# Kernel tuning notes

Hardware: AMD Instinct MI355X
Metric: run time of the kernel (lower is better)

The kernel has to match this reference:

```python
import jax, jax.numpy as jnp
import numpy as np

K, D, S, H = 8, 2, 1, 12  # kernel_size, dilation, stride, h_size


def setup_inputs() -> dict:
    key = jax.random.key(0)
    k1, k2 = jax.random.split(key)
    x = jax.random.normal(k1, (32, 2048, 64), dtype=jnp.float32)
    A = jax.random.normal(k2, (64, H, H), dtype=jnp.float32) * 0.1
    return {"x": x, "A": A}


def reference(x, A):
    B, T, C = x.shape
    pad = (K + (K - 1) * (D - 1) - 1) // 2  # = 7
    # replicate padding along time
    xp = jnp.pad(x, ((0, 0), (pad, pad), (0, 0)), mode='edge')  # (B, Tp, C)
    Tp = xp.shape[1]
    seg = (Tp - (K - 1) * D - 1) // S + 1
    # dilated unfold: gather overlapping windows along time
    idx = jnp.arange(seg)[:, None] * S + jnp.arange(K)[None, :] * D  # (seg, K)
    win = xp[:, idx, :]                       # (B, seg, K, C)
    w = win.reshape(B * seg, K, C)            # (N, K, C)
    # path increments within each window
    dx = w[:, 1:, :] - w[:, :-1, :]           # (N, K-1, C)
    # skew-symmetric (so(n)) parametrisation of the Lie-algebra map
    Ask = A - jnp.swapaxes(A, -1, -2)         # (C, H, H)
    M = jnp.einsum('nkc,chw->nkhw', dx, Ask)  # (N, K-1, H, H)
    # matrix exponential of each increment's Lie-algebra element
    E = jax.vmap(jax.scipy.linalg.expm)(M.reshape(-1, H, H)).reshape(M.shape)
    # sequential development: z_{t+1} = z_t @ exp(M_t), z_0 = I
    z0 = jnp.broadcast_to(jnp.eye(H, dtype=x.dtype), (B * seg, H, H))

    def step(z, e):
        return jnp.matmul(z, e), None

    zT, _ = jax.lax.scan(step, z0, jnp.swapaxes(E, 0, 1))  # scan over K-1 steps
    dev = zT.reshape(B, seg, H * H)
    sp = w[:, 0, :].reshape(B, seg, C)        # start point of each partition
    return jnp.concatenate([dev, sp], axis=-1)  # (B, seg, H*H + C)
```

## Files before the change

### kernel.cpp

```cpp
#include <hip/hip_runtime.h>

#define B_ 32
#define T_ 2048
#define C_ 64
#define NP_ 2060
#define MSTRIDE 144
#define LSTRIDE 148

typedef short short8_t __attribute__((ext_vector_type(8)));
typedef float f32x4 __attribute__((ext_vector_type(4)));

__device__ __forceinline__ unsigned short f2bf(float f) {
  unsigned u = __float_as_uint(f);
  return (unsigned short)((u + 0x7FFFu + ((u >> 16) & 1u)) >> 16);
}
__device__ __forceinline__ float bf2f(unsigned short s) {
  return __uint_as_float(((unsigned)s) << 16);
}

__global__ __launch_bounds__(256) void k1_mfma(const float* __restrict__ x,
                                               const float* __restrict__ A,
                                               float* __restrict__ M) {
  __shared__ unsigned int askw[9216];
  const int b = blockIdx.y;
  const int p0 = blockIdx.x * 64;
  const int tid = threadIdx.x;
  const float sc = 1.0f / 32.0f;

  for (int P = tid; P < 4608; P += 256) {
    const int j2 = P & 3;
    const int col = (P >> 2) & 15;
    const int koct = (P >> 6) & 3;
    const int rest = P >> 8;
    const int tile = rest % 9;
    const int ks = rest / 9;
    const int e = tile * 16 + col;
    const int h = e / 12, w = e - h * 12;
    const int c0 = ks * 32 + koct * 8 + j2 * 2;
    const float v0 = (A[c0 * 144 + e] - A[c0 * 144 + w * 12 + h]) * sc;
    const float v1 = (A[(c0 + 1) * 144 + e] - A[(c0 + 1) * 144 + w * 12 + h]) * sc;
    const unsigned short h0 = f2bf(v0), h1 = f2bf(v1);
    const unsigned short l0 = f2bf(v0 - bf2f(h0)), l1 = f2bf(v1 - bf2f(h1));
    const int widx = (((ks * 9 + tile) * 4 + koct) * 16 + col) * 4 + j2;
    askw[widx] = ((unsigned)h1 << 16) | h0;
    askw[4608 + widx] = ((unsigned)l1 << 16) | l0;
  }
  __syncthreads();

  const int wv = tid >> 6;
  const int lane = tid & 63;
  const int mrow = lane & 15;
  const int koct = lane >> 4;
  const int p = p0 + wv * 16 + mrow;
  const int i1 = min(max(p - 7, 0), T_ - 1);
  const int i2 = min(max(p - 5, 0), T_ - 1);
  const float* xb = x + (size_t)b * T_ * C_;

  short8_t ah[2], al[2];
#pragma unroll
  for (int ks = 0; ks < 2; ++ks) {
    const int c0 = ks * 32 + koct * 8;
    const float4 u1a = *(const float4*)(xb + (size_t)i1 * C_ + c0);
    const float4 u1b = *(const float4*)(xb + (size_t)i1 * C_ + c0 + 4);
    const float4 u2a = *(const float4*)(xb + (size_t)i2 * C_ + c0);
    const float4 u2b = *(const float4*)(xb + (size_t)i2 * C_ + c0 + 4);
    float d[8];
    d[0] = u2a.x - u1a.x; d[1] = u2a.y - u1a.y;
    d[2] = u2a.z - u1a.z; d[3] = u2a.w - u1a.w;
    d[4] = u2b.x - u1b.x; d[5] = u2b.y - u1b.y;
    d[6] = u2b.z - u1b.z; d[7] = u2b.w - u1b.w;
#pragma unroll
    for (int j = 0; j < 8; ++j) {
      const unsigned short hs = f2bf(d[j]);
      ah[ks][j] = (short)hs;
      al[ks][j] = (short)f2bf(d[j] - bf2f(hs));
    }
  }

  float* Mb = M + (size_t)b * NP_ * MSTRIDE;
  const int dcol = lane & 15;
  const int pbase = p0 + wv * 16 + (lane >> 4) * 4;
  const char* lds = (const char*)askw;
#pragma unroll
  for (int tile = 0; tile < 9; ++tile) {
    f32x4 acc = {0.f, 0.f, 0.f, 0.f};
#pragma unroll
    for (int ks = 0; ks < 2; ++ks) {
      const int fb = (((ks * 9 + tile) * 4 + koct) * 16 + dcol) * 16;
      const short8_t bh = *(const short8_t*)(lds + fb);
      const short8_t bl = *(const short8_t*)(lds + 18432 + fb);
      acc = __builtin_amdgcn_mfma_f32_16x16x32_bf16(ah[ks], bh, acc, 0, 0, 0);
      acc = __builtin_amdgcn_mfma_f32_16x16x32_bf16(ah[ks], bl, acc, 0, 0, 0);
      acc = __builtin_amdgcn_mfma_f32_16x16x32_bf16(al[ks], bh, acc, 0, 0, 0);
    }
#pragma unroll
    for (int reg = 0; reg < 4; ++reg) {
      const int pr = pbase + reg;
      if (pr < NP_) Mb[(size_t)pr * MSTRIDE + tile * 16 + dcol] = acc[reg];
    }
  }
}

template <int Q>
__device__ __forceinline__ float qb(float v) {
  return __int_as_float(
      __builtin_amdgcn_mov_dpp(__float_as_int(v), Q * 0x55, 0xf, 0xf, true));
}

template <bool ACC>
__device__ __forceinline__ void qmm_t(const float a[3][12], const float b[3][12],
                                      float c[3][12]) {
  if (!ACC) {
#pragma unroll
    for (int i = 0; i < 3; ++i)
#pragma unroll
      for (int j = 0; j < 12; ++j) c[i][j] = 0.f;
  }
#define QMM_K(OWNER, E)                                                  \
  {                                                                      \
    float bk[12];                                                        \
    _Pragma("unroll")                                                    \
    for (int j = 0; j < 12; ++j) bk[j] = qb<OWNER>(b[E][j]);             \
    _Pragma("unroll")                                                    \
    for (int i = 0; i < 3; ++i) {                                        \
      const float av = a[i][3 * OWNER + E];                              \
      _Pragma("unroll")                                                  \
      for (int j = 0; j < 12; ++j) c[i][j] = fmaf(av, bk[j], c[i][j]);   \
    }                                                                    \
  }
  QMM_K(0, 0) QMM_K(0, 1) QMM_K(0, 2)
  QMM_K(1, 0) QMM_K(1, 1) QMM_K(1, 2)
  QMM_K(2, 0) QMM_K(2, 1) QMM_K(2, 2)
  QMM_K(3, 0) QMM_K(3, 1) QMM_K(3, 2)
#undef QMM_K
}
__device__ __forceinline__ void qmm(const float a[3][12], const float b[3][12],
                                    float c[3][12]) { qmm_t<false>(a, b, c); }
__device__ __forceinline__ void qmma(const float a[3][12], const float b[3][12],
                                     float c[3][12]) { qmm_t<true>(a, b, c); }

__global__ __launch_bounds__(256) void k2_expm(float* __restrict__ M) {
  const int gq = (blockIdx.x * 256 + threadIdx.x) >> 2;
  const int r = threadIdx.x & 3;
  float* gp = M + (size_t)gq * MSTRIDE + 36 * r;

  float a[3][12], t2[3][12], t3[3][12];
#pragma unroll
  for (int i = 0; i < 3; ++i)
#pragma unroll
    for (int q4 = 0; q4 < 3; ++q4) {
      float4 v = *(const float4*)(gp + i * 12 + q4 * 4);
      a[i][q4 * 4 + 0] = v.x;
      a[i][q4 * 4 + 1] = v.y;
      a[i][q4 * 4 + 2] = v.z;
      a[i][q4 * 4 + 3] = v.w;
    }

  qmm(a, a, t2);
  qmm(t2, a, t3);
#pragma unroll
  for (int i = 0; i < 3; ++i)
#pragma unroll
    for (int j = 0; j < 12; ++j) {
      const float av = a[i][j], t2v = t2[i][j], t3v = t3[i][j];
      t2[i][j] = av + t2v * 0.5f + t3v * (1.0f / 6.0f) +
                 ((j == 3 * r + i) ? 1.0f : 0.0f);
      a[i][j] = av * (1.0f / 24.0f) + t2v * (1.0f / 120.0f) +
                t3v * (1.0f / 720.0f);
    }
  qmma(t3, a, t2);

  qmm(t2, t2, t3);
  qmm(t3, t3, t2);
  qmm(t2, t2, t3);
  qmm(t3, t3, t2);
  qmm(t2, t2, t3);

#pragma unroll
  for (int i = 0; i < 3; ++i)
#pragma unroll
    for (int q4 = 0; q4 < 3; ++q4)
      *(float4*)(gp + i * 12 + q4 * 4) =
          make_float4(t3[i][q4 * 4 + 0], t3[i][q4 * 4 + 1],
                      t3[i][q4 * 4 + 2], t3[i][q4 * 4 + 3]);
}

__global__ __launch_bounds__(256) void k3_chain(const float* __restrict__ E,
                                                const float* __restrict__ x,
                                                float* __restrict__ out) {
  __shared__ float eb[76][LSTRIDE];
  const int b = blockIdx.y;
  const int t0 = blockIdx.x * 64;
  const float* src = E + ((size_t)b * NP_ + t0) * MSTRIDE;
  for (int i = threadIdx.x; i < 76 * 36; i += 256) {
    int m = i / 36, q = i - m * 36;
    *(float4*)(&eb[m][q * 4]) = *(const float4*)(src + (size_t)m * MSTRIDE + q * 4);
  }
  __syncthreads();

  const int r = threadIdx.x & 3;
  const int tl = threadIdx.x >> 2;
  const int t = t0 + tl;

  float z[3][12], c[3][12];
#pragma unroll
  for (int i = 0; i < 3; ++i) {
    const float* zp = &eb[tl][(3 * r + i) * 12];
    float4 v0 = *(const float4*)(zp + 0);
    float4 v1 = *(const float4*)(zp + 4);
    float4 v2 = *(const float4*)(zp + 8);
    z[i][0] = v0.x; z[i][1] = v0.y; z[i][2]  = v0.z; z[i][3]  = v0.w;
    z[i][4] = v1.x; z[i][5] = v1.y; z[i][6]  = v1.z; z[i][7]  = v1.w;
    z[i][8] = v2.x; z[i][9] = v2.y; z[i][10] = v2.z; z[i][11] = v2.w;
  }

#define CHAIN_STEP(SRC, DST, J)                                          \
  {                                                                      \
    float bb[3][12];                                                     \
    _Pragma("unroll")                                                    \
    for (int i = 0; i < 3; ++i) {                                        \
      const float* ep = &eb[tl + 2 * (J)][(3 * r + i) * 12];             \
      float4 v0 = *(const float4*)(ep + 0);                              \
      float4 v1 = *(const float4*)(ep + 4);                              \
      float4 v2 = *(const float4*)(ep + 8);                              \
      bb[i][0] = v0.x; bb[i][1] = v0.y; bb[i][2]  = v0.z; bb[i][3]  = v0.w; \
      bb[i][4] = v1.x; bb[i][5] = v1.y; bb[i][6]  = v1.z; bb[i][7]  = v1.w; \
      bb[i][8] = v2.x; bb[i][9] = v2.y; bb[i][10] = v2.z; bb[i][11] = v2.w; \
    }                                                                    \
    qmm(SRC, bb, DST);                                                   \
  }
  CHAIN_STEP(z, c, 1)
  CHAIN_STEP(c, z, 2)
  CHAIN_STEP(z, c, 3)
  CHAIN_STEP(c, z, 4)
  CHAIN_STEP(z, c, 5)
  CHAIN_STEP(c, z, 6)
#undef CHAIN_STEP

  const size_t obase = ((size_t)b * T_ + t) * 208;
#pragma unroll
  for (int i = 0; i < 3; ++i) {
    const int row = 3 * r + i;
    *(float4*)(out + obase + row * 12 + 0) = make_float4(z[i][0], z[i][1], z[i][2],  z[i][3]);
    *(float4*)(out + obase + row * 12 + 4) = make_float4(z[i][4], z[i][5], z[i][6],  z[i][7]);
    *(float4*)(out + obase + row * 12 + 8) = make_float4(z[i][8], z[i][9], z[i][10], z[i][11]);
  }
  const int xi = min(max(t - 7, 0), T_ - 1);
  const float* xr = x + ((size_t)b * T_ + xi) * C_ + 16 * r;
#pragma unroll
  for (int q = 0; q < 4; ++q) {
    *(float4*)(out + obase + 144 + 16 * r + q * 4) = *(const float4*)(xr + q * 4);
  }
}

extern "C" void kernel_launch(void* const* d_in, const int* in_sizes, int n_in,
                              void* d_out, int out_size, void* d_ws, size_t ws_size,
                              hipStream_t stream) {
  (void)in_sizes; (void)n_in; (void)out_size;
  const float* x = (const float*)d_in[0];
  const float* A = (const float*)d_in[1];
  float* out = (float*)d_out;
  float* M = (float*)d_ws;

  const size_t need = (size_t)B_ * NP_ * MSTRIDE * sizeof(float);
  if (ws_size < need) return;

  k1_mfma<<<dim3(33, B_), 256, 0, stream>>>(x, A, M);
  k2_expm<<<dim3((B_ * NP_ * 4) / 256), 256, 0, stream>>>(M);
  k3_chain<<<dim3(T_ / 64, B_), 256, 0, stream>>>(M, x, out);
}
```

Baseline: 109.8 us.

## Share middle chain product between outputs two steps apart in chain kernel

Outputs t and t+2 share five middle matrix factors (E[t+2..t+12] with stride 2). Each thread now computes that shared product once and finishes both outputs with one extra multiply each, so the 6 multiplies per output drop to about 3.5. To fit this, blocks cover 96 timesteps with 192 active threads, leaving a quarter of each block idle. Shared-memory staging grows to 110 rows, with clamped reads past the end.

```diff
diff --git a/kernel.cpp b/kernel.cpp
--- a/kernel.cpp
+++ b/kernel.cpp
@@ -6,6 +6,8 @@
 #define NP_ 2060
 #define MSTRIDE 144
 #define LSTRIDE 148
+#define W3_ 96
+#define NE3_ 110
 
 typedef short short8_t __attribute__((ext_vector_type(8)));
 typedef float f32x4 __attribute__((ext_vector_type(4)));
@@ -185,72 +187,77 @@
                       t3[i][q4 * 4 + 2], t3[i][q4 * 4 + 3]);
 }
 
-__global__ __launch_bounds__(256) void k3_chain(const float* __restrict__ E,
-                                                const float* __restrict__ x,
-                                                float* __restrict__ out) {
-  __shared__ float eb[76][LSTRIDE];
+__global__ __launch_bounds__(256) void k3_pair(const float* __restrict__ E,
+                                               const float* __restrict__ x,
+                                               float* __restrict__ out) {
+  __shared__ float eb[NE3_][LSTRIDE];
   const int b = blockIdx.y;
-  const int t0 = blockIdx.x * 64;
-  const float* src = E + ((size_t)b * NP_ + t0) * MSTRIDE;
-  for (int i = threadIdx.x; i < 76 * 36; i += 256) {
-    int m = i / 36, q = i - m * 36;
-    *(float4*)(&eb[m][q * 4]) = *(const float4*)(src + (size_t)m * MSTRIDE + q * 4);
+  const int t0 = blockIdx.x * W3_;
+  const float* src = E + (size_t)b * NP_ * MSTRIDE;
+  for (int i = threadIdx.x; i < NE3_ * 36; i += 256) {
+    const int m = i / 36, q = i - m * 36;
+    const int p = min(t0 + m, NP_ - 1);
+    *(float4*)(&eb[m][q * 4]) = *(const float4*)(src + (size_t)p * MSTRIDE + q * 4);
   }
   __syncthreads();
 
   const int r = threadIdx.x & 3;
-  const int tl = threadIdx.x >> 2;
-  const int t = t0 + tl;
-
-  float z[3][12], c[3][12];
-#pragma unroll
-  for (int i = 0; i < 3; ++i) {
-    const float* zp = &eb[tl][(3 * r + i) * 12];
-    float4 v0 = *(const float4*)(zp + 0);
-    float4 v1 = *(const float4*)(zp + 4);
-    float4 v2 = *(const float4*)(zp + 8);
-    z[i][0] = v0.x; z[i][1] = v0.y; z[i][2]  = v0.z; z[i][3]  = v0.w;
-    z[i][4] = v1.x; z[i][5] = v1.y; z[i][6]  = v1.z; z[i][7]  = v1.w;
-    z[i][8] = v2.x; z[i][9] = v2.y; z[i][10] = v2.z; z[i][11] = v2.w;
-  }
-
-#define CHAIN_STEP(SRC, DST, J)                                          \
+  const int pr = threadIdx.x >> 2;
+  if (pr >= 48) return;
+  const int par = pr & 1, jj = pr >> 1;
+  const int tloc = 4 * jj + par;
+  const int t1 = t0 + tloc;
+
+#define LOADB(DST, IDX)                                                  \
   {                                                                      \
-    float bb[3][12];                                                     \
     _Pragma("unroll")                                                    \
     for (int i = 0; i < 3; ++i) {                                        \
-      const float* ep = &eb[tl + 2 * (J)][(3 * r + i) * 12];             \
+      const float* ep = &eb[(IDX)][(3 * r + i) * 12];                    \
       float4 v0 = *(const float4*)(ep + 0);                              \
       float4 v1 = *(const float4*)(ep + 4);                              \
       float4 v2 = *(const float4*)(ep + 8);                              \
-      bb[i][0] = v0.x; bb[i][1] = v0.y; bb[i][2]  = v0.z; bb[i][3]  = v0.w; \
-      bb[i][4] = v1.x; bb[i][5] = v1.y; bb[i][6]  = v1.z; bb[i][7]  = v1.w; \
-      bb[i][8] = v2.x; bb[i][9] = v2.y; bb[i][10] = v2.z; bb[i][11] = v2.w; \
-    }                                                                    \
-    qmm(SRC, bb, DST);                                                   \
-  }
-  CHAIN_STEP(z, c, 1)
-  CHAIN_STEP(c, z, 2)
-  CHAIN_STEP(z, c, 3)
-  CHAIN_STEP(c, z, 4)
-  CHAIN_STEP(z, c, 5)
-  CHAIN_STEP(c, z, 6)
-#undef CHAIN_STEP
-
-  const size_t obase = ((size_t)b * T_ + t) * 208;
-#pragma unroll
-  for (int i = 0; i < 3; ++i) {
-    const int row = 3 * r + i;
-    *(float4*)(out + obase + row * 12 + 0) = make_float4(z[i][0], z[i][1], z[i][2],  z[i][3]);
-    *(float4*)(out + obase + row * 12 + 4) = make_float4(z[i][4], z[i][5], z[i][6],  z[i][7]);
-    *(float4*)(out + obase + row * 12 + 8) = make_float4(z[i][8], z[i][9], z[i][10], z[i][11]);
-  }
-  const int xi = min(max(t - 7, 0), T_ - 1);
-  const float* xr = x + ((size_t)b * T_ + xi) * C_ + 16 * r;
-#pragma unroll
-  for (int q = 0; q < 4; ++q) {
-    *(float4*)(out + obase + 144 + 16 * r + q * 4) = *(const float4*)(xr + q * 4);
-  }
+      DST[i][0] = v0.x; DST[i][1] = v0.y; DST[i][2]  = v0.z; DST[i][3]  = v0.w; \
+      DST[i][4] = v1.x; DST[i][5] = v1.y; DST[i][6]  = v1.z; DST[i][7]  = v1.w; \
+      DST[i][8] = v2.x; DST[i][9] = v2.y; DST[i][10] = v2.z; DST[i][11] = v2.w; \
+    }                                                                    \
+  }
+
+#define STOREZ(SRCZ, TW)                                                 \
+  {                                                                      \
+    const size_t obase = ((size_t)b * T_ + (TW)) * 208;                  \
+    _Pragma("unroll")                                                    \
+    for (int i = 0; i < 3; ++i) {                                        \
+      const int row = 3 * r + i;                                         \
+      *(float4*)(out + obase + row * 12 + 0) =                           \
+          make_float4(SRCZ[i][0], SRCZ[i][1], SRCZ[i][2],  SRCZ[i][3]);  \
+      *(float4*)(out + obase + row * 12 + 4) =                           \
+          make_float4(SRCZ[i][4], SRCZ[i][5], SRCZ[i][6],  SRCZ[i][7]);  \
+      *(float4*)(out + obase + row * 12 + 8) =                           \
+          make_float4(SRCZ[i][8], SRCZ[i][9], SRCZ[i][10], SRCZ[i][11]); \
+    }                                                                    \
+    const int xi = min(max((TW) - 7, 0), T_ - 1);                        \
+    const float* xr = x + ((size_t)b * T_ + xi) * C_ + 16 * r;           \
+    _Pragma("unroll")                                                    \
+    for (int qd = 0; qd < 4; ++qd) {                                     \
+      *(float4*)(out + obase + 144 + 16 * r + qd * 4) =                  \
+          *(const float4*)(xr + qd * 4);                                 \
+    }                                                                    \
+  }
+
+  float rr[3][12], cc[3][12], bb[3][12];
+  LOADB(rr, tloc + 2);
+  LOADB(bb, tloc + 4);  qmm(rr, bb, cc);
+  LOADB(bb, tloc + 6);  qmm(cc, bb, rr);
+  LOADB(bb, tloc + 8);  qmm(rr, bb, cc);
+  LOADB(bb, tloc + 10); qmm(cc, bb, rr);
+  LOADB(bb, tloc + 12); qmm(rr, bb, cc);
+
+  LOADB(bb, tloc);      qmm(bb, cc, rr);
+  if (t1 < T_) STOREZ(rr, t1);
+  LOADB(bb, tloc + 14); qmm(cc, bb, rr);
+  if (t1 + 2 < T_) STOREZ(rr, t1 + 2);
+#undef LOADB
+#undef STOREZ
 }
 
 extern "C" void kernel_launch(void* const* d_in, const int* in_sizes, int n_in,
@@ -267,5 +274,5 @@
 
   k1_mfma<<<dim3(33, B_), 256, 0, stream>>>(x, A, M);
   k2_expm<<<dim3((B_ * NP_ * 4) / 256), 256, 0, stream>>>(M);
-  k3_chain<<<dim3(T_ / 64, B_), 256, 0, stream>>>(M, x, out);
-}
+  k3_pair<<<dim3((T_ + W3_ - 1) / W3_, B_), 256, 0, stream>>>(M, x, out);
+}
```

New measurement: 122.0 us. 1.11x slower.

## Fuse Lie-algebra MFMA projection and matrix exponential into one kernel

Applied to the files above, without the earlier changes.

The MFMA kernel that builds the 12x12 increment matrices and the expm kernel are merged. The M tiles now stay in shared memory (reusing the Ask staging buffer) and go straight into the squaring-based exponential. This removes a full global write and read of the M workspace and one kernel launch. In exchange the fused kernel needs more registers and LDS per block, plus extra barriers, which may lower occupancy.

```diff
diff --git a/kernel.cpp b/kernel.cpp
--- a/kernel.cpp
+++ b/kernel.cpp
@@ -6,6 +6,7 @@
 #define NP_ 2060
 #define MSTRIDE 144
 #define LSTRIDE 148
+#define MBS 148
 
 typedef short short8_t __attribute__((ext_vector_type(8)));
 typedef float f32x4 __attribute__((ext_vector_type(4)));
@@ -18,10 +19,49 @@
   return __uint_as_float(((unsigned)s) << 16);
 }
 
-__global__ __launch_bounds__(256) void k1_mfma(const float* __restrict__ x,
-                                               const float* __restrict__ A,
-                                               float* __restrict__ M) {
-  __shared__ unsigned int askw[9216];
+template <int Q>
+__device__ __forceinline__ float qb(float v) {
+  return __int_as_float(
+      __builtin_amdgcn_mov_dpp(__float_as_int(v), Q * 0x55, 0xf, 0xf, true));
+}
+
+template <bool ACC>
+__device__ __forceinline__ void qmm_t(const float a[3][12], const float b[3][12],
+                                      float c[3][12]) {
+  if (!ACC) {
+#pragma unroll
+    for (int i = 0; i < 3; ++i)
+#pragma unroll
+      for (int j = 0; j < 12; ++j) c[i][j] = 0.f;
+  }
+#define QMM_K(OWNER, E)                                                  \
+  {                                                                      \
+    float bk[12];                                                        \
+    _Pragma("unroll")                                                    \
+    for (int j = 0; j < 12; ++j) bk[j] = qb<OWNER>(b[E][j]);             \
+    _Pragma("unroll")                                                    \
+    for (int i = 0; i < 3; ++i) {                                        \
+      const float av = a[i][3 * OWNER + E];                              \
+      _Pragma("unroll")                                                  \
+      for (int j = 0; j < 12; ++j) c[i][j] = fmaf(av, bk[j], c[i][j]);   \
+    }                                                                    \
+  }
+  QMM_K(0, 0) QMM_K(0, 1) QMM_K(0, 2)
+  QMM_K(1, 0) QMM_K(1, 1) QMM_K(1, 2)
+  QMM_K(2, 0) QMM_K(2, 1) QMM_K(2, 2)
+  QMM_K(3, 0) QMM_K(3, 1) QMM_K(3, 2)
+#undef QMM_K
+}
+__device__ __forceinline__ void qmm(const float a[3][12], const float b[3][12],
+                                    float c[3][12]) { qmm_t<false>(a, b, c); }
+__device__ __forceinline__ void qmma(const float a[3][12], const float b[3][12],
+                                     float c[3][12]) { qmm_t<true>(a, b, c); }
+
+__global__ __launch_bounds__(256) void k12_fused(const float* __restrict__ x,
+                                                 const float* __restrict__ A,
+                                                 float* __restrict__ E) {
+  __shared__ float smem[64 * MBS];
+  unsigned int* askw = (unsigned int*)smem;
   const int b = blockIdx.y;
   const int p0 = blockIdx.x * 64;
   const int tid = threadIdx.x;
@@ -45,116 +85,84 @@
     askw[widx] = ((unsigned)h1 << 16) | h0;
     askw[4608 + widx] = ((unsigned)l1 << 16) | l0;
   }
-  __syncthreads();
 
   const int wv = tid >> 6;
   const int lane = tid & 63;
   const int mrow = lane & 15;
   const int koct = lane >> 4;
-  const int p = p0 + wv * 16 + mrow;
-  const int i1 = min(max(p - 7, 0), T_ - 1);
-  const int i2 = min(max(p - 5, 0), T_ - 1);
-  const float* xb = x + (size_t)b * T_ * C_;
-
-  short8_t ah[2], al[2];
-#pragma unroll
-  for (int ks = 0; ks < 2; ++ks) {
-    const int c0 = ks * 32 + koct * 8;
-    const float4 u1a = *(const float4*)(xb + (size_t)i1 * C_ + c0);
-    const float4 u1b = *(const float4*)(xb + (size_t)i1 * C_ + c0 + 4);
-    const float4 u2a = *(const float4*)(xb + (size_t)i2 * C_ + c0);
-    const float4 u2b = *(const float4*)(xb + (size_t)i2 * C_ + c0 + 4);
-    float d[8];
-    d[0] = u2a.x - u1a.x; d[1] = u2a.y - u1a.y;
-    d[2] = u2a.z - u1a.z; d[3] = u2a.w - u1a.w;
-    d[4] = u2b.x - u1b.x; d[5] = u2b.y - u1b.y;
-    d[6] = u2b.z - u1b.z; d[7] = u2b.w - u1b.w;
-#pragma unroll
-    for (int j = 0; j < 8; ++j) {
-      const unsigned short hs = f2bf(d[j]);
-      ah[ks][j] = (short)hs;
-      al[ks][j] = (short)f2bf(d[j] - bf2f(hs));
-    }
-  }
-
-  float* Mb = M + (size_t)b * NP_ * MSTRIDE;
-  const int dcol = lane & 15;
-  const int pbase = p0 + wv * 16 + (lane >> 4) * 4;
-  const char* lds = (const char*)askw;
-#pragma unroll
-  for (int tile = 0; tile < 9; ++tile) {
-    f32x4 acc = {0.f, 0.f, 0.f, 0.f};
+  {
+    const int p = p0 + wv * 16 + mrow;
+    const int i1 = min(max(p - 7, 0), T_ - 1);
+    const int i2 = min(max(p - 5, 0), T_ - 1);
+    const float* xb = x + (size_t)b * T_ * C_;
+    short8_t ah[2], al[2];
 #pragma unroll
     for (int ks = 0; ks < 2; ++ks) {
-      const int fb = (((ks * 9 + tile) * 4 + koct) * 16 + dcol) * 16;
-      const short8_t bh = *(const short8_t*)(lds + fb);
-      const short8_t bl = *(const short8_t*)(lds + 18432 + fb);
-      acc = __builtin_amdgcn_mfma_f32_16x16x32_bf16(ah[ks], bh, acc, 0, 0, 0);
-      acc = __builtin_amdgcn_mfma_f32_16x16x32_bf16(ah[ks], bl, acc, 0, 0, 0);
-      acc = __builtin_amdgcn_mfma_f32_16x16x32_bf16(al[ks], bh, acc, 0, 0, 0);
-    }
+      const int c0 = ks * 32 + koct * 8;
+      const float4 u1a = *(const float4*)(xb + (size_t)i1 * C_ + c0);
+      const float4 u1b = *(const float4*)(xb + (size_t)i1 * C_ + c0 + 4);
+      const float4 u2a = *(const float4*)(xb + (size_t)i2 * C_ + c0);
+      const float4 u2b = *(const float4*)(xb + (size_t)i2 * C_ + c0 + 4);
+      float d[8];
+      d[0] = u2a.x - u1a.x; d[1] = u2a.y - u1a.y;
+      d[2] = u2a.z - u1a.z; d[3] = u2a.w - u1a.w;
+      d[4] = u2b.x - u1b.x; d[5] = u2b.y - u1b.y;
+      d[6] = u2b.z - u1b.z; d[7] = u2b.w - u1b.w;
+#pragma unroll
+      for (int j = 0; j < 8; ++j) {
+        const unsigned short hs = f2bf(d[j]);
+        ah[ks][j] = (short)hs;
+        al[ks][j] = (short)f2bf(d[j] - bf2f(hs));
+      }
+    }
+    __syncthreads();
+
+    f32x4 accs[9];
+    const int dcol = lane & 15;
+    const char* lds = (const char*)askw;
+#pragma unroll
+    for (int tile = 0; tile < 9; ++tile) {
+      f32x4 acc = {0.f, 0.f, 0.f, 0.f};
+#pragma unroll
+      for (int ks = 0; ks < 2; ++ks) {
+        const int fb = (((ks * 9 + tile) * 4 + koct) * 16 + dcol) * 16;
+        const short8_t bh = *(const short8_t*)(lds + fb);
+        const short8_t bl = *(const short8_t*)(lds + 18432 + fb);
+        acc = __builtin_amdgcn_mfma_f32_16x16x32_bf16(ah[ks], bh, acc, 0, 0, 0);
+        acc = __builtin_amdgcn_mfma_f32_16x16x32_bf16(ah[ks], bl, acc, 0, 0, 0);
+        acc = __builtin_amdgcn_mfma_f32_16x16x32_bf16(al[ks], bh, acc, 0, 0, 0);
+      }
+      accs[tile] = acc;
+    }
+    __syncthreads();
+
+    const int nlbase = wv * 16 + (lane >> 4) * 4;
 #pragma unroll
     for (int reg = 0; reg < 4; ++reg) {
-      const int pr = pbase + reg;
-      if (pr < NP_) Mb[(size_t)pr * MSTRIDE + tile * 16 + dcol] = acc[reg];
-    }
-  }
-}
-
-template <int Q>
-__device__ __forceinline__ float qb(float v) {
-  return __int_as_float(
-      __builtin_amdgcn_mov_dpp(__float_as_int(v), Q * 0x55, 0xf, 0xf, true));
-}
-
-template <bool ACC>
-__device__ __forceinline__ void qmm_t(const float a[3][12], const float b[3][12],
-                                      float c[3][12]) {
-  if (!ACC) {
-#pragma unroll
-    for (int i = 0; i < 3; ++i)
-#pragma unroll
-      for (int j = 0; j < 12; ++j) c[i][j] = 0.f;
-  }
-#define QMM_K(OWNER, E)                                                  \
-  {                                                                      \
-    float bk[12];                                                        \
-    _Pragma("unroll")                                                    \
-    for (int j = 0; j < 12; ++j) bk[j] = qb<OWNER>(b[E][j]);             \
-    _Pragma("unroll")                                                    \
-    for (int i = 0; i < 3; ++i) {                                        \
-      const float av = a[i][3 * OWNER + E];                              \
-      _Pragma("unroll")                                                  \
-      for (int j = 0; j < 12; ++j) c[i][j] = fmaf(av, bk[j], c[i][j]);   \
-    }                                                                    \
-  }
-  QMM_K(0, 0) QMM_K(0, 1) QMM_K(0, 2)
-  QMM_K(1, 0) QMM_K(1, 1) QMM_K(1, 2)
-  QMM_K(2, 0) QMM_K(2, 1) QMM_K(2, 2)
-  QMM_K(3, 0) QMM_K(3, 1) QMM_K(3, 2)
-#undef QMM_K
-}
-__device__ __forceinline__ void qmm(const float a[3][12], const float b[3][12],
-                                    float c[3][12]) { qmm_t<false>(a, b, c); }
-__device__ __forceinline__ void qmma(const float a[3][12], const float b[3][12],
-                                     float c[3][12]) { qmm_t<true>(a, b, c); }
-
-__global__ __launch_bounds__(256) void k2_expm(float* __restrict__ M) {
-  const int gq = (blockIdx.x * 256 + threadIdx.x) >> 2;
-  const int r = threadIdx.x & 3;
-  float* gp = M + (size_t)gq * MSTRIDE + 36 * r;
-
+      float* mrow_ = smem + (nlbase + reg) * MBS;
+#pragma unroll
+      for (int tile = 0; tile < 9; ++tile)
+        mrow_[tile * 16 + dcol] = accs[tile][reg];
+    }
+  }
+  __syncthreads();
+
+  const int q = tid >> 2;
+  const int r = tid & 3;
   float a[3][12], t2[3][12], t3[3][12];
-#pragma unroll
-  for (int i = 0; i < 3; ++i)
-#pragma unroll
-    for (int q4 = 0; q4 < 3; ++q4) {
-      float4 v = *(const float4*)(gp + i * 12 + q4 * 4);
-      a[i][q4 * 4 + 0] = v.x;
-      a[i][q4 * 4 + 1] = v.y;
-      a[i][q4 * 4 + 2] = v.z;
-      a[i][q4 * 4 + 3] = v.w;
-    }
+  {
+    const float* mp = smem + q * MBS;
+#pragma unroll
+    for (int i = 0; i < 3; ++i) {
+      const float* rp = mp + (3 * r + i) * 12;
+      float4 v0 = *(const float4*)(rp + 0);
+      float4 v1 = *(const float4*)(rp + 4);
+      float4 v2 = *(const float4*)(rp + 8);
+      a[i][0] = v0.x; a[i][1] = v0.y; a[i][2]  = v0.z; a[i][3]  = v0.w;
+      a[i][4] = v1.x; a[i][5] = v1.y; a[i][6]  = v1.z; a[i][7]  = v1.w;
+      a[i][8] = v2.x; a[i][9] = v2.y; a[i][10] = v2.z; a[i][11] = v2.w;
+    }
+  }
 
   qmm(a, a, t2);
   qmm(t2, a, t3);
@@ -176,13 +184,17 @@
   qmm(t3, t3, t2);
   qmm(t2, t2, t3);
 
-#pragma unroll
-  for (int i = 0; i < 3; ++i)
-#pragma unroll
-    for (int q4 = 0; q4 < 3; ++q4)
-      *(float4*)(gp + i * 12 + q4 * 4) =
-          make_float4(t3[i][q4 * 4 + 0], t3[i][q4 * 4 + 1],
-                      t3[i][q4 * 4 + 2], t3[i][q4 * 4 + 3]);
+  const int p = p0 + q;
+  if (p < NP_) {
+    float* gp = E + ((size_t)b * NP_ + p) * MSTRIDE + 36 * r;
+#pragma unroll
+    for (int i = 0; i < 3; ++i)
+#pragma unroll
+      for (int q4 = 0; q4 < 3; ++q4)
+        *(float4*)(gp + i * 12 + q4 * 4) =
+            make_float4(t3[i][q4 * 4 + 0], t3[i][q4 * 4 + 1],
+                        t3[i][q4 * 4 + 2], t3[i][q4 * 4 + 3]);
+  }
 }
 
 __global__ __launch_bounds__(256) void k3_chain(const float* __restrict__ E,
@@ -260,12 +272,11 @@
   const float* x = (const float*)d_in[0];
   const float* A = (const float*)d_in[1];
   float* out = (float*)d_out;
-  float* M = (float*)d_ws;
+  float* E = (float*)d_ws;
 
   const size_t need = (size_t)B_ * NP_ * MSTRIDE * sizeof(float);
   if (ws_size < need) return;
 
-  k1_mfma<<<dim3(33, B_), 256, 0, stream>>>(x, A, M);
-  k2_expm<<<dim3((B_ * NP_ * 4) / 256), 256, 0, stream>>>(M);
-  k3_chain<<<dim3(T_ / 64, B_), 256, 0, stream>>>(M, x, out);
-}
+  k12_fused<<<dim3(33, B_), 256, 0, stream>>>(x, A, E);
+  k3_chain<<<dim3(T_ / 64, B_), 256, 0, stream>>>(E, x, out);
+}
```

Result: slower. 123.4 us (+12.4%).
